# Kernel tuning notes

Measured on AMD Instinct MI355X. Metric: run time of the kernel, lower is better.

## Reference

```python
import jax, jax.numpy as jnp
import numpy as np

HIDDEN = 512
D = 2 * HIDDEN  # 1024


def setup_inputs() -> dict:
    key = jax.random.key(0)
    ks = jax.random.split(key, 7)
    B, S = 8, 2048
    scale = 1.0 / np.sqrt(D)
    return {
        "lstm_out": jax.random.normal(ks[0], (B, S, D), dtype=jnp.float32),
        "Wq": jax.random.normal(ks[1], (D, D), dtype=jnp.float32) * scale,
        "bq": jnp.zeros((D,), dtype=jnp.float32),
        "Wk": jax.random.normal(ks[2], (D, D), dtype=jnp.float32) * scale,
        "bk": jnp.zeros((D,), dtype=jnp.float32),
        "Wv": jax.random.normal(ks[3], (D, D), dtype=jnp.float32) * scale,
        "bv": jnp.zeros((D,), dtype=jnp.float32),
    }


def reference(lstm_out, Wq, bq, Wk, bk, Wv, bv):
    # Q, K, V: [B, S, D]
    Q = jnp.einsum("bsd,de->bse", lstm_out, Wq) + bq
    K = jnp.einsum("bsd,de->bse", lstm_out, Wk) + bk
    V = jnp.einsum("bsd,de->bse", lstm_out, Wv) + bv
    # NOTE: original module has no 1/sqrt(d) scaling
    scores = jnp.einsum("bqd,bkd->bqk", Q, K)  # [B, S, S]
    weights = jax.nn.softmax(scores, axis=-1)
    context = jnp.einsum("bqk,bkd->bqd", weights, V)  # [B, S, D]
    return context
```

## Files before the change

kernel.cpp:

```cpp
#include <hip/hip_runtime.h>
#include <hip/hip_bf16.h>

static constexpr int S = 2048;
static constexpr int D = 1024;
static constexpr int NB = 8;

#define LOG2E 1.4426950408889634f

typedef float    f32x4  __attribute__((ext_vector_type(4)));
typedef _Float16 f16x4  __attribute__((ext_vector_type(4)));
typedef _Float16 f16x8  __attribute__((ext_vector_type(8)));

#define CM_F32    0
#define CM_SPLIT  1
#define CM_TRANSV 2
#define CM_F16    3

#define GLD16(g, l) __builtin_amdgcn_global_load_lds(                         \
    (const __attribute__((address_space(1))) void*)(g),                       \
    (__attribute__((address_space(3))) void*)(l), 16, 0, 0)

#define MFMA16(a, b, c) __builtin_amdgcn_mfma_f32_16x16x32_f16((a), (b), (c), 0, 0, 0)
#define BAR() __builtin_amdgcn_s_barrier()
#define PRIO1() __builtin_amdgcn_s_setprio(1)
#define PRIO0() __builtin_amdgcn_s_setprio(0)
#define WAIT_LGKM(n) asm volatile("s_waitcnt lgkmcnt(" #n ")" ::: "memory")
#define WAIT_VM(n)   asm volatile("s_waitcnt vmcnt(" #n ")" ::: "memory")

template <int TERMS, int CMODE, int BNT>
__global__ __launch_bounds__(512, 1) void bgemm256(
    const _Float16* __restrict__ Ah_, const _Float16* __restrict__ Al_, long sAz,
    const _Float16* __restrict__ Bh_, const _Float16* __restrict__ Bl_, long sBz,
    int lda, int ldb,
    void* __restrict__ C1, void* __restrict__ C2, int ldc, long sCz,
    const float* __restrict__ bias, int K)
{
    extern __shared__ char smem[];
    constexpr int NW_N  = BNT / 64;
    constexpr int NW_M  = 8 / NW_N;
    constexpr int WM    = 256 / NW_M;
    constexpr int MI    = WM / 16;
    constexpr int APLANE = 16384;
    constexpr int BPLANE = BNT * 64;
    constexpr int NAP    = (TERMS == 2) ? 1 : 2;
    constexpr int BOFF   = NAP * APLANE;
    constexpr int BUFSZ  = NAP * APLANE + 2 * BPLANE;

    int bx, by, bz;
    {
        const int gx = gridDim.x, gy = gridDim.y;
        const int nwg = gx * gy * gridDim.z;
        const int wg = blockIdx.x + gx * (blockIdx.y + gy * blockIdx.z);
        const int q = nwg >> 3, r = nwg & 7;
        const int xcd = wg & 7, i = wg >> 3;
        const int nid = (xcd < r) ? xcd * (q + 1) + i
                                  : r * (q + 1) + (xcd - r) * q + i;
        bx = nid % gx;
        const int tmp = nid / gx;
        by = tmp % gy;
        bz = tmp / gy;
    }

    const int t = threadIdx.x;
    const int z = bz;
    const int m0 = by * 256;
    const int n0 = bx * BNT;
    const int lane = t & 63, wid = t >> 6;
    const int wr = wid / NW_N, wc = wid % NW_N;
    const int fr = lane & 15, fq = lane >> 4;
    const int lrow = lane >> 2, lslot = lane & 3;

    const _Float16* Ahz = Ah_ + (long)z * sAz;
    const _Float16* Bhz = Bh_ + (long)z * sBz;
    const _Float16* Blz = (TERMS == 2) ? Bl_ + (long)z * sBz : nullptr;

    auto stA = [&](int tile, int p) {
        const _Float16* plane = Ahz;
        char* lbase = smem + (tile & 1) * BUFSZ + p * APLANE;
#pragma unroll
        for (int i = 0; i < 2; ++i) {
            const int row = wid * 32 + i * 16 + lrow;
            const int chunk = lslot ^ ((row >> 1) & 3);
            const long kk = (TERMS == 1) ? (long)tile * 64 + p * 32 + chunk * 8
                                         : (long)tile * 32 + chunk * 8;
            GLD16(plane + (long)(m0 + row) * lda + kk,
                  lbase + (wid * 32 + i * 16) * 64);
        }
    };
    auto stB = [&](int tile, int p) {
        const _Float16* plane = (TERMS == 2 && p) ? Blz : Bhz;
        char* lbase = smem + (tile & 1) * BUFSZ + BOFF + p * BPLANE;
        if (TERMS == 2) {
#pragma unroll
            for (int i = 0; i < 2; ++i) {
                const int row = wid * 32 + i * 16 + lrow;
                const int chunk = lslot ^ ((row >> 1) & 3);
                const long kk = (long)tile * 32 + chunk * 8;
                GLD16(plane + (long)(n0 + row) * ldb + kk,
                      lbase + (wid * 32 + i * 16) * 64);
            }
        } else {
            const int row = wid * 16 + lrow;
            const int chunk = lslot ^ ((row >> 1) & 3);
            const long kk = (long)tile * 64 + p * 32 + chunk * 8;
            GLD16(plane + (long)(n0 + row) * ldb + kk, lbase + (wid * 16) * 64);
        }
    };
    auto rdA = [&](int buf, int p, int mi) -> f16x8 {
        const int row = wr * WM + mi * 16 + fr;
        const int slot = fq ^ ((row >> 1) & 3);
        return *(const f16x8*)(smem + buf * BUFSZ + p * APLANE +
                               row * 64 + slot * 16);
    };
    auto rdB = [&](int buf, int p, int ni) -> f16x8 {
        const int row = wc * 64 + ni * 16 + fr;
        const int slot = fq ^ ((row >> 1) & 3);
        return *(const f16x8*)(smem + buf * BUFSZ + BOFF + p * BPLANE +
                               row * 64 + slot * 16);
    };

    f32x4 acc[MI][4] = {};
    const int ktiles = K / ((TERMS == 1) ? 64 : 32);

    if constexpr (TERMS == 2) {
        f16x8 b0h[4], b0l[4], aA[4], aB[4];
        auto mb = [&](int base, f16x8 (&A)[4], f16x8 (&B)[4]) {
#pragma unroll
            for (int mi = 0; mi < 4; ++mi)
#pragma unroll
                for (int ni = 0; ni < 4; ++ni)
                    acc[base + mi][ni] = MFMA16(A[mi], B[ni], acc[base + mi][ni]);
        };
        stA(0, 0); stB(0, 0); stB(0, 1);
        WAIT_VM(0);
        BAR();
#pragma unroll
        for (int ni = 0; ni < 4; ++ni) b0h[ni] = rdB(0, 0, ni);
#pragma unroll
        for (int mi = 0; mi < 4; ++mi) aA[mi] = rdA(0, 0, mi);
#pragma unroll
        for (int mi = 0; mi < 4; ++mi) aB[mi] = rdA(0, 0, 4 + mi);

        for (int tt = 0; tt < ktiles; ++tt) {
            const int buf = tt & 1;
            const bool pf = (tt + 1 < ktiles);
            if (pf) { stA(tt + 1, 0); stB(tt + 1, 0); WAIT_VM(4); }
            else    { WAIT_VM(0); }
            BAR();
            WAIT_LGKM(4);
            PRIO1(); mb(0, aA, b0h); PRIO0();
            if (pf) stB(tt + 1, 1);
#pragma unroll
            for (int ni = 0; ni < 4; ++ni) b0l[ni] = rdB(buf, 1, ni);
            WAIT_LGKM(4);
            PRIO1(); mb(4, aB, b0h); PRIO0();
            if (pf) WAIT_VM(2);
            BAR();
            WAIT_LGKM(0);
            PRIO1(); mb(0, aA, b0l); PRIO0();
            PRIO1(); mb(4, aB, b0l); PRIO0();
            if (pf) {
                const int nb = buf ^ 1;
#pragma unroll
                for (int ni = 0; ni < 4; ++ni) b0h[ni] = rdB(nb, 0, ni);
#pragma unroll
                for (int mi = 0; mi < 4; ++mi) aA[mi] = rdA(nb, 0, mi);
#pragma unroll
                for (int mi = 0; mi < 4; ++mi) aB[mi] = rdA(nb, 0, 4 + mi);
            }
            BAR();
        }
    } else {
        f16x8 b0[4], b1[4], a0[4], a1[4];
        auto mb = [&](f16x8 (&A)[4], f16x8 (&B)[4]) {
#pragma unroll
            for (int mi = 0; mi < 4; ++mi)
#pragma unroll
                for (int ni = 0; ni < 4; ++ni)
                    acc[mi][ni] = MFMA16(A[mi], B[ni], acc[mi][ni]);
        };
        stA(0, 0); stB(0, 0); stA(0, 1); stB(0, 1);
        WAIT_VM(0);
        BAR();
#pragma unroll
        for (int ni = 0; ni < 4; ++ni) b0[ni] = rdB(0, 0, ni);
#pragma unroll
        for (int mi = 0; mi < 4; ++mi) a0[mi] = rdA(0, 0, mi);

        for (int tt = 0; tt < ktiles; ++tt) {
            const int buf = tt & 1;
            const bool pf = (tt + 1 < ktiles);
            if (pf) { stA(tt + 1, 0); stB(tt + 1, 0); WAIT_VM(3); }
            else    { WAIT_VM(0); }
            BAR();
#pragma unroll
            for (int ni = 0; ni < 4; ++ni) b1[ni] = rdB(buf, 1, ni);
#pragma unroll
            for (int mi = 0; mi < 4; ++mi) a1[mi] = rdA(buf, 1, mi);
            WAIT_LGKM(8);
            PRIO1(); mb(a0, b0); PRIO0();
            BAR();
            if (pf) { stA(tt + 1, 1); stB(tt + 1, 1); WAIT_VM(3); }
            WAIT_LGKM(0);
            BAR();
            PRIO1(); mb(a1, b1); PRIO0();
            if (pf) {
                const int nb = buf ^ 1;
#pragma unroll
                for (int ni = 0; ni < 4; ++ni) b0[ni] = rdB(nb, 0, ni);
#pragma unroll
                for (int mi = 0; mi < 4; ++mi) a0[mi] = rdA(nb, 0, mi);
            }
        }
    }

#pragma unroll
    for (int mi = 0; mi < MI; ++mi) {
        const int rbase = m0 + wr * WM + mi * 16 + fq * 4;
#pragma unroll
        for (int ni = 0; ni < 4; ++ni) {
            const int col = n0 + wc * 64 + ni * 16 + fr;
            f32x4 a = acc[mi][ni];
            if (CMODE != CM_F32) {
                const float bv = bias[col];
#pragma unroll
                for (int j = 0; j < 4; ++j) a[j] += bv;
            }
            if (CMODE == CM_F32) {
                float* C = (float*)C1 + (long)z * sCz;
#pragma unroll
                for (int j = 0; j < 4; ++j)
                    C[(long)(rbase + j) * ldc + col] = a[j];
            } else if (CMODE == CM_F16) {
                _Float16* Ch = (_Float16*)C1;
#pragma unroll
                for (int j = 0; j < 4; ++j)
                    Ch[(long)(rbase + j) * ldc + col] = (_Float16)a[j];
            } else if (CMODE == CM_SPLIT) {
                _Float16* Ch = (_Float16*)C1;
                _Float16* Cl = (_Float16*)C2;
#pragma unroll
                for (int j = 0; j < 4; ++j) {
                    const float q = a[j];
                    const _Float16 h = (_Float16)q;
                    Ch[(long)(rbase + j) * ldc + col] = h;
                    Cl[(long)(rbase + j) * ldc + col] = (_Float16)(q - (float)h);
                }
            } else {
                const int b_ = rbase >> 11;
                const int s_ = rbase & (S - 1);
                f16x4 h;
#pragma unroll
                for (int j = 0; j < 4; ++j) h[j] = (_Float16)a[j];
                *(f16x4*)((_Float16*)C1 + ((long)b_ * D + col) * S + s_) = h;
            }
        }
    }
}

__global__ __launch_bounds__(256) void xsplit(
    const float* __restrict__ X, _Float16* __restrict__ Xh)
{
    const long i = ((long)blockIdx.x * 256 + threadIdx.x) * 8;
    f32x4 v0 = *(const f32x4*)(X + i);
    f32x4 v1 = *(const f32x4*)(X + i + 4);
    f16x8 h;
#pragma unroll
    for (int j = 0; j < 4; ++j) { h[j] = (_Float16)v0[j]; h[4 + j] = (_Float16)v1[j]; }
    *(f16x8*)(Xh + i) = h;
}

__global__ void wsplit(const float* __restrict__ W0, const float* __restrict__ W1,
                       const float* __restrict__ W2, _Float16* __restrict__ Th)
{
    const float* W = blockIdx.z == 0 ? W0 : (blockIdx.z == 1 ? W1 : W2);
    _Float16* th = Th + (long)blockIdx.z * 1024 * 1024;
    __shared__ float tile[32][33];
    const int bx = blockIdx.x * 32, by = blockIdx.y * 32;
    const int tx = threadIdx.x, ty = threadIdx.y;
#pragma unroll
    for (int i = ty; i < 32; i += 8) tile[i][tx] = W[(long)(by + i) * 1024 + bx + tx];
    __syncthreads();
#pragma unroll
    for (int i = ty; i < 32; i += 8)
        th[(long)(bx + i) * 1024 + by + tx] = (_Float16)tile[tx][i];
}

__global__ __launch_bounds__(256) void pconv(float* __restrict__ Sb)
{
    const long row = blockIdx.x;
    float* p = Sb + row * (long)S;
    const int t = threadIdx.x;

    f32x4 x0 = *(const f32x4*)(p + t * 8);
    f32x4 x1 = *(const f32x4*)(p + t * 8 + 4);

    float m = -3.4e38f;
#pragma unroll
    for (int j = 0; j < 4; ++j) m = fmaxf(m, fmaxf(x0[j], x1[j]));
#pragma unroll
    for (int o = 32; o >= 1; o >>= 1) m = fmaxf(m, __shfl_xor(m, o));

    __shared__ float wm[4], wsum[4];
    const int wid = t >> 6, lane = t & 63;
    if (lane == 0) wm[wid] = m;
    __syncthreads();
    m = fmaxf(fmaxf(wm[0], wm[1]), fmaxf(wm[2], wm[3]));

    float e[8], ssum = 0.f;
#pragma unroll
    for (int j = 0; j < 4; ++j) {
        e[j]     = exp2f((x0[j] - m) * LOG2E);
        e[4 + j] = exp2f((x1[j] - m) * LOG2E);
        ssum += e[j] + e[4 + j];
    }
#pragma unroll
    for (int o = 32; o >= 1; o >>= 1) ssum += __shfl_xor(ssum, o);
    if (lane == 0) wsum[wid] = ssum;
    __syncthreads();
    const float invl = 1.0f / (wsum[0] + wsum[1] + wsum[2] + wsum[3]);

    f16x8 outv;
#pragma unroll
    for (int j = 0; j < 8; ++j) outv[j] = (_Float16)(e[j] * invl);
    *(f16x8*)((_Float16*)p + t * 8) = outv;
}

extern "C" void kernel_launch(void* const* d_in, const int* in_sizes, int n_in,
                              void* d_out, int out_size, void* d_ws, size_t ws_size,
                              hipStream_t stream)
{
    const float* X  = (const float*)d_in[0];
    const float* Wq = (const float*)d_in[1];
    const float* bq = (const float*)d_in[2];
    const float* Wk = (const float*)d_in[3];
    const float* bk = (const float*)d_in[4];
    const float* Wv = (const float*)d_in[5];
    const float* bv = (const float*)d_in[6];
    float* out = (float*)d_out;
    char* ws = (char*)d_ws;
    const size_t MB = 1u << 20;

    _Float16* Wh = (_Float16*)ws;
    _Float16* Qh = (_Float16*)(ws + 12 * MB);
    _Float16* Kh = (_Float16*)(ws + 76 * MB);
    _Float16* Vt = (_Float16*)(ws + 140 * MB);
    float*    Sb = (float*)(ws + 172 * MB);
    _Float16* Xh = (_Float16*)(ws + 172 * MB);

    const int LDS_T1 = 98304;
    hipFuncSetAttribute(reinterpret_cast<const void*>(&bgemm256<1, CM_F16, 128>),
                        hipFuncAttributeMaxDynamicSharedMemorySize, LDS_T1);
    hipFuncSetAttribute(reinterpret_cast<const void*>(&bgemm256<1, CM_TRANSV, 128>),
                        hipFuncAttributeMaxDynamicSharedMemorySize, LDS_T1);
    hipFuncSetAttribute(reinterpret_cast<const void*>(&bgemm256<1, CM_F32, 128>),
                        hipFuncAttributeMaxDynamicSharedMemorySize, LDS_T1);

    xsplit<<<dim3(8192), 256, 0, stream>>>(X, Xh);
    wsplit<<<dim3(32, 32, 3), dim3(32, 8), 0, stream>>>(Wq, Wk, Wv, Wh);

    const long MW = 1024 * 1024;
    bgemm256<1, CM_F16, 128><<<dim3(D / 128, 64, 1), 512, LDS_T1, stream>>>(
        Xh, nullptr, 0, Wh, nullptr, 0, D, D, Qh, nullptr, D, 0, bq, D);
    bgemm256<1, CM_F16, 128><<<dim3(D / 128, 64, 1), 512, LDS_T1, stream>>>(
        Xh, nullptr, 0, Wh + MW, nullptr, 0, D, D, Kh, nullptr, D, 0, bk, D);
    bgemm256<1, CM_TRANSV, 128><<<dim3(D / 128, 64, 1), 512, LDS_T1, stream>>>(
        Xh, nullptr, 0, Wh + 2 * MW, nullptr, 0, D, D, Vt, nullptr, 0, 0, bv, D);

    for (int g = 0; g < 2; ++g) {
        const int b0 = g * 4;
        bgemm256<1, CM_F32, 128><<<dim3(S / 128, S / 256, 4), 512, LDS_T1, stream>>>(
            Qh + (long)b0 * S * D, nullptr, (long)S * D,
            Kh + (long)b0 * S * D, nullptr, (long)S * D,
            D, D, Sb, nullptr, S, (long)S * S, nullptr, D);
        pconv<<<dim3(4 * S), 256, 0, stream>>>(Sb);
        bgemm256<1, CM_F32, 128><<<dim3(D / 128, S / 256, 4), 512, LDS_T1, stream>>>(
            (const _Float16*)Sb, nullptr, 2L * S * S,
            Vt + (long)b0 * D * S, nullptr, (long)D * S,
            2 * S, S, out + (long)b0 * S * D, nullptr, D, (long)S * D, nullptr, S);
    }
}
```

Before: 377.6 us.

## Stage transposed V epilogue through LDS and batch all attention in single launches

Drops the unused two-term split-precision path and templates. The transposed-V epilogue now writes tiles into shared memory and stores 16-byte rows to global, replacing scattered 8-byte column writes. The score GEMM, softmax conversion and PV GEMM now each run once over all 8 batches instead of in two groups of 4. This roughly doubles the score buffer footprint and shrinks the workspace offsets, so the larger buffer must still fit in the workspace.

Measured after the change: 362.5 us. 4.0% less time.

```diff
diff --git a/kernel.cpp b/kernel.cpp
--- a/kernel.cpp
+++ b/kernel.cpp
@@ -12,7 +12,6 @@
 typedef _Float16 f16x8  __attribute__((ext_vector_type(8)));
 
 #define CM_F32    0
-#define CM_SPLIT  1
 #define CM_TRANSV 2
 #define CM_F16    3
 
@@ -27,24 +26,22 @@
 #define WAIT_LGKM(n) asm volatile("s_waitcnt lgkmcnt(" #n ")" ::: "memory")
 #define WAIT_VM(n)   asm volatile("s_waitcnt vmcnt(" #n ")" ::: "memory")
 
-template <int TERMS, int CMODE, int BNT>
+template <int CMODE>
 __global__ __launch_bounds__(512, 1) void bgemm256(
-    const _Float16* __restrict__ Ah_, const _Float16* __restrict__ Al_, long sAz,
-    const _Float16* __restrict__ Bh_, const _Float16* __restrict__ Bl_, long sBz,
+    const _Float16* __restrict__ Ah_, long sAz,
+    const _Float16* __restrict__ Bh_, long sBz,
     int lda, int ldb,
-    void* __restrict__ C1, void* __restrict__ C2, int ldc, long sCz,
+    void* __restrict__ C1, int ldc, long sCz,
     const float* __restrict__ bias, int K)
 {
     extern __shared__ char smem[];
-    constexpr int NW_N  = BNT / 64;
-    constexpr int NW_M  = 8 / NW_N;
-    constexpr int WM    = 256 / NW_M;
-    constexpr int MI    = WM / 16;
+    constexpr int BNT   = 128;
+    constexpr int WM    = 64;
+    constexpr int MI    = 4;
     constexpr int APLANE = 16384;
     constexpr int BPLANE = BNT * 64;
-    constexpr int NAP    = (TERMS == 2) ? 1 : 2;
-    constexpr int BOFF   = NAP * APLANE;
-    constexpr int BUFSZ  = NAP * APLANE + 2 * BPLANE;
+    constexpr int BOFF   = 2 * APLANE;
+    constexpr int BUFSZ  = 2 * APLANE + 2 * BPLANE;
 
     int bx, by, bz;
     {
@@ -66,45 +63,30 @@
     const int m0 = by * 256;
     const int n0 = bx * BNT;
     const int lane = t & 63, wid = t >> 6;
-    const int wr = wid / NW_N, wc = wid % NW_N;
+    const int wr = wid >> 1, wc = wid & 1;
     const int fr = lane & 15, fq = lane >> 4;
     const int lrow = lane >> 2, lslot = lane & 3;
 
     const _Float16* Ahz = Ah_ + (long)z * sAz;
     const _Float16* Bhz = Bh_ + (long)z * sBz;
-    const _Float16* Blz = (TERMS == 2) ? Bl_ + (long)z * sBz : nullptr;
 
     auto stA = [&](int tile, int p) {
-        const _Float16* plane = Ahz;
         char* lbase = smem + (tile & 1) * BUFSZ + p * APLANE;
 #pragma unroll
         for (int i = 0; i < 2; ++i) {
             const int row = wid * 32 + i * 16 + lrow;
             const int chunk = lslot ^ ((row >> 1) & 3);
-            const long kk = (TERMS == 1) ? (long)tile * 64 + p * 32 + chunk * 8
-                                         : (long)tile * 32 + chunk * 8;
-            GLD16(plane + (long)(m0 + row) * lda + kk,
+            const long kk = (long)tile * 64 + p * 32 + chunk * 8;
+            GLD16(Ahz + (long)(m0 + row) * lda + kk,
                   lbase + (wid * 32 + i * 16) * 64);
         }
     };
     auto stB = [&](int tile, int p) {
-        const _Float16* plane = (TERMS == 2 && p) ? Blz : Bhz;
         char* lbase = smem + (tile & 1) * BUFSZ + BOFF + p * BPLANE;
-        if (TERMS == 2) {
-#pragma unroll
-            for (int i = 0; i < 2; ++i) {
-                const int row = wid * 32 + i * 16 + lrow;
-                const int chunk = lslot ^ ((row >> 1) & 3);
-                const long kk = (long)tile * 32 + chunk * 8;
-                GLD16(plane + (long)(n0 + row) * ldb + kk,
-                      lbase + (wid * 32 + i * 16) * 64);
-            }
-        } else {
-            const int row = wid * 16 + lrow;
-            const int chunk = lslot ^ ((row >> 1) & 3);
-            const long kk = (long)tile * 64 + p * 32 + chunk * 8;
-            GLD16(plane + (long)(n0 + row) * ldb + kk, lbase + (wid * 16) * 64);
-        }
+        const int row = wid * 16 + lrow;
+        const int chunk = lslot ^ ((row >> 1) & 3);
+        const long kk = (long)tile * 64 + p * 32 + chunk * 8;
+        GLD16(Bhz + (long)(n0 + row) * ldb + kk, lbase + (wid * 16) * 64);
     };
     auto rdA = [&](int buf, int p, int mi) -> f16x8 {
         const int row = wr * WM + mi * 16 + fr;
@@ -120,57 +102,9 @@
     };
 
     f32x4 acc[MI][4] = {};
-    const int ktiles = K / ((TERMS == 1) ? 64 : 32);
-
-    if constexpr (TERMS == 2) {
-        f16x8 b0h[4], b0l[4], aA[4], aB[4];
-        auto mb = [&](int base, f16x8 (&A)[4], f16x8 (&B)[4]) {
-#pragma unroll
-            for (int mi = 0; mi < 4; ++mi)
-#pragma unroll
-                for (int ni = 0; ni < 4; ++ni)
-                    acc[base + mi][ni] = MFMA16(A[mi], B[ni], acc[base + mi][ni]);
-        };
-        stA(0, 0); stB(0, 0); stB(0, 1);
-        WAIT_VM(0);
-        BAR();
-#pragma unroll
-        for (int ni = 0; ni < 4; ++ni) b0h[ni] = rdB(0, 0, ni);
-#pragma unroll
-        for (int mi = 0; mi < 4; ++mi) aA[mi] = rdA(0, 0, mi);
-#pragma unroll
-        for (int mi = 0; mi < 4; ++mi) aB[mi] = rdA(0, 0, 4 + mi);
-
-        for (int tt = 0; tt < ktiles; ++tt) {
-            const int buf = tt & 1;
-            const bool pf = (tt + 1 < ktiles);
-            if (pf) { stA(tt + 1, 0); stB(tt + 1, 0); WAIT_VM(4); }
-            else    { WAIT_VM(0); }
-            BAR();
-            WAIT_LGKM(4);
-            PRIO1(); mb(0, aA, b0h); PRIO0();
-            if (pf) stB(tt + 1, 1);
-#pragma unroll
-            for (int ni = 0; ni < 4; ++ni) b0l[ni] = rdB(buf, 1, ni);
-            WAIT_LGKM(4);
-            PRIO1(); mb(4, aB, b0h); PRIO0();
-            if (pf) WAIT_VM(2);
-            BAR();
-            WAIT_LGKM(0);
-            PRIO1(); mb(0, aA, b0l); PRIO0();
-            PRIO1(); mb(4, aB, b0l); PRIO0();
-            if (pf) {
-                const int nb = buf ^ 1;
-#pragma unroll
-                for (int ni = 0; ni < 4; ++ni) b0h[ni] = rdB(nb, 0, ni);
-#pragma unroll
-                for (int mi = 0; mi < 4; ++mi) aA[mi] = rdA(nb, 0, mi);
-#pragma unroll
-                for (int mi = 0; mi < 4; ++mi) aB[mi] = rdA(nb, 0, 4 + mi);
-            }
-            BAR();
-        }
-    } else {
+    const int ktiles = K / 64;
+
+    {
         f16x8 b0[4], b1[4], a0[4], a1[4];
         auto mb = [&](f16x8 (&A)[4], f16x8 (&B)[4]) {
 #pragma unroll
@@ -214,45 +148,56 @@
         }
     }
 
-#pragma unroll
-    for (int mi = 0; mi < MI; ++mi) {
-        const int rbase = m0 + wr * WM + mi * 16 + fq * 4;
-#pragma unroll
-        for (int ni = 0; ni < 4; ++ni) {
-            const int col = n0 + wc * 64 + ni * 16 + fr;
-            f32x4 a = acc[mi][ni];
-            if (CMODE != CM_F32) {
-                const float bv = bias[col];
-#pragma unroll
-                for (int j = 0; j < 4; ++j) a[j] += bv;
+    if constexpr (CMODE == CM_TRANSV) {
+        constexpr int LDT = 544;
+#pragma unroll
+        for (int mi = 0; mi < MI; ++mi) {
+            const int row0 = wr * WM + mi * 16 + fq * 4;
+#pragma unroll
+            for (int ni = 0; ni < 4; ++ni) {
+                const int colp = wc * 64 + ni * 16 + fr;
+                const float bv = bias[n0 + colp];
+                f16x4 h;
+#pragma unroll
+                for (int j = 0; j < 4; ++j) h[j] = (_Float16)(acc[mi][ni][j] + bv);
+                *(f16x4*)(smem + colp * LDT + row0 * 2) = h;
             }
-            if (CMODE == CM_F32) {
-                float* C = (float*)C1 + (long)z * sCz;
-#pragma unroll
-                for (int j = 0; j < 4; ++j)
-                    C[(long)(rbase + j) * ldc + col] = a[j];
-            } else if (CMODE == CM_F16) {
-                _Float16* Ch = (_Float16*)C1;
-#pragma unroll
-                for (int j = 0; j < 4; ++j)
-                    Ch[(long)(rbase + j) * ldc + col] = (_Float16)a[j];
-            } else if (CMODE == CM_SPLIT) {
-                _Float16* Ch = (_Float16*)C1;
-                _Float16* Cl = (_Float16*)C2;
-#pragma unroll
-                for (int j = 0; j < 4; ++j) {
-                    const float q = a[j];
-                    const _Float16 h = (_Float16)q;
-                    Ch[(long)(rbase + j) * ldc + col] = h;
-                    Cl[(long)(rbase + j) * ldc + col] = (_Float16)(q - (float)h);
+        }
+        BAR();
+        const int b_ = m0 >> 11;
+        const int sbase = m0 & (S - 1);
+        const int l31 = lane & 31, lh = lane >> 5;
+        _Float16* Vp = (_Float16*)C1;
+#pragma unroll
+        for (int it = 0; it < 8; ++it) {
+            const int dd = wid * 16 + it * 2 + lh;
+            const f16x8 v = *(const f16x8*)(smem + dd * LDT + l31 * 16);
+            *(f16x8*)(Vp + ((long)(b_ * D + n0 + dd)) * S + sbase + l31 * 8) = v;
+        }
+    } else {
+#pragma unroll
+        for (int mi = 0; mi < MI; ++mi) {
+            const int rbase = m0 + wr * WM + mi * 16 + fq * 4;
+#pragma unroll
+            for (int ni = 0; ni < 4; ++ni) {
+                const int col = n0 + wc * 64 + ni * 16 + fr;
+                f32x4 a = acc[mi][ni];
+                if (CMODE != CM_F32) {
+                    const float bv = bias[col];
+#pragma unroll
+                    for (int j = 0; j < 4; ++j) a[j] += bv;
                 }
-            } else {
-                const int b_ = rbase >> 11;
-                const int s_ = rbase & (S - 1);
-                f16x4 h;
-#pragma unroll
-                for (int j = 0; j < 4; ++j) h[j] = (_Float16)a[j];
-                *(f16x4*)((_Float16*)C1 + ((long)b_ * D + col) * S + s_) = h;
+                if (CMODE == CM_F32) {
+                    float* C = (float*)C1 + (long)z * sCz;
+#pragma unroll
+                    for (int j = 0; j < 4; ++j)
+                        C[(long)(rbase + j) * ldc + col] = a[j];
+                } else {
+                    _Float16* Ch = (_Float16*)C1;
+#pragma unroll
+                    for (int j = 0; j < 4; ++j)
+                        Ch[(long)(rbase + j) * ldc + col] = (_Float16)a[j];
+                }
             }
         }
     }
@@ -342,41 +287,36 @@
     const size_t MB = 1u << 20;
 
     _Float16* Wh = (_Float16*)ws;
-    _Float16* Qh = (_Float16*)(ws + 12 * MB);
-    _Float16* Kh = (_Float16*)(ws + 76 * MB);
-    _Float16* Vt = (_Float16*)(ws + 140 * MB);
-    float*    Sb = (float*)(ws + 172 * MB);
-    _Float16* Xh = (_Float16*)(ws + 172 * MB);
+    _Float16* Qh = (_Float16*)(ws + 6 * MB);
+    _Float16* Kh = (_Float16*)(ws + 38 * MB);
+    _Float16* Vt = (_Float16*)(ws + 70 * MB);
+    float*    Sb = (float*)(ws + 102 * MB);
+    _Float16* Xh = (_Float16*)(ws + 102 * MB);
 
     const int LDS_T1 = 98304;
-    hipFuncSetAttribute(reinterpret_cast<const void*>(&bgemm256<1, CM_F16, 128>),
+    hipFuncSetAttribute(reinterpret_cast<const void*>(&bgemm256<CM_F16>),
                         hipFuncAttributeMaxDynamicSharedMemorySize, LDS_T1);
-    hipFuncSetAttribute(reinterpret_cast<const void*>(&bgemm256<1, CM_TRANSV, 128>),
+    hipFuncSetAttribute(reinterpret_cast<const void*>(&bgemm256<CM_TRANSV>),
                         hipFuncAttributeMaxDynamicSharedMemorySize, LDS_T1);
-    hipFuncSetAttribute(reinterpret_cast<const void*>(&bgemm256<1, CM_F32, 128>),
+    hipFuncSetAttribute(reinterpret_cast<const void*>(&bgemm256<CM_F32>),
                         hipFuncAttributeMaxDynamicSharedMemorySize, LDS_T1);
 
     xsplit<<<dim3(8192), 256, 0, stream>>>(X, Xh);
     wsplit<<<dim3(32, 32, 3), dim3(32, 8), 0, stream>>>(Wq, Wk, Wv, Wh);
 
     const long MW = 1024 * 1024;
-    bgemm256<1, CM_F16, 128><<<dim3(D / 128, 64, 1), 512, LDS_T1, stream>>>(
-        Xh, nullptr, 0, Wh, nullptr, 0, D, D, Qh, nullptr, D, 0, bq, D);
-    bgemm256<1, CM_F16, 128><<<dim3(D / 128, 64, 1), 512, LDS_T1, stream>>>(
-        Xh, nullptr, 0, Wh + MW, nullptr, 0, D, D, Kh, nullptr, D, 0, bk, D);
-    bgemm256<1, CM_TRANSV, 128><<<dim3(D / 128, 64, 1), 512, LDS_T1, stream>>>(
-        Xh, nullptr, 0, Wh + 2 * MW, nullptr, 0, D, D, Vt, nullptr, 0, 0, bv, D);
-
-    for (int g = 0; g < 2; ++g) {
-        const int b0 = g * 4;
-        bgemm256<1, CM_F32, 128><<<dim3(S / 128, S / 256, 4), 512, LDS_T1, stream>>>(
-            Qh + (long)b0 * S * D, nullptr, (long)S * D,
-            Kh + (long)b0 * S * D, nullptr, (long)S * D,
-            D, D, Sb, nullptr, S, (long)S * S, nullptr, D);
-        pconv<<<dim3(4 * S), 256, 0, stream>>>(Sb);
-        bgemm256<1, CM_F32, 128><<<dim3(D / 128, S / 256, 4), 512, LDS_T1, stream>>>(
-            (const _Float16*)Sb, nullptr, 2L * S * S,
-            Vt + (long)b0 * D * S, nullptr, (long)D * S,
-            2 * S, S, out + (long)b0 * S * D, nullptr, D, (long)S * D, nullptr, S);
-    }
-}
+    bgemm256<CM_F16><<<dim3(D / 128, 64, 1), 512, LDS_T1, stream>>>(
+        Xh, 0, Wh, 0, D, D, Qh, D, 0, bq, D);
+    bgemm256<CM_F16><<<dim3(D / 128, 64, 1), 512, LDS_T1, stream>>>(
+        Xh, 0, Wh + MW, 0, D, D, Kh, D, 0, bk, D);
+    bgemm256<CM_TRANSV><<<dim3(D / 128, 64, 1), 512, LDS_T1, stream>>>(
+        Xh, 0, Wh + 2 * MW, 0, D, D, Vt, 0, 0, bv, D);
+
+    bgemm256<CM_F32><<<dim3(S / 128, S / 256, NB), 512, LDS_T1, stream>>>(
+        Qh, (long)S * D, Kh, (long)S * D,
+        D, D, Sb, S, (long)S * S, nullptr, D);
+    pconv<<<dim3(NB * S), 256, 0, stream>>>(Sb);
+    bgemm256<CM_F32><<<dim3(D / 128, S / 256, NB), 512, LDS_T1, stream>>>(
+        (const _Float16*)Sb, 2L * S * S, Vt, (long)D * S,
+        2 * S, S, out, D, (long)S * D, nullptr, S);
+}
```
